# Optimization experiments

Measured on AMD Instinct MI355X. Metric: run time of the kernel, lower is better.

## Reference

```python
import jax, jax.numpy as jnp
import numpy as np

CH = 128
GROUPS = 8
HEADS = 8
HEAD_DIM = CH // HEADS  # 16
EPS = 1e-5


def setup_inputs() -> dict:
    key = jax.random.key(0)
    ks = jax.random.split(key, 5)
    x = jax.random.normal(ks[0], (8, CH, 128, 128), dtype=jnp.float32)
    gn_w = jnp.ones((CH,), dtype=jnp.float32)
    gn_b = jnp.zeros((CH,), dtype=jnp.float32)
    w_in = jax.random.normal(ks[1], (CH, CH), dtype=jnp.float32) * (1.0 / np.sqrt(CH))
    b_in = jax.random.normal(ks[2], (CH,), dtype=jnp.float32) * 0.01
    w_out = jax.random.normal(ks[3], (CH, CH), dtype=jnp.float32) * (1.0 / np.sqrt(CH))
    b_out = jax.random.normal(ks[4], (CH,), dtype=jnp.float32) * 0.01
    return {"x": x, "gn_w": gn_w, "gn_b": gn_b, "w_in": w_in, "b_in": b_in,
            "w_out": w_out, "b_out": b_out}


def _group_norm(x, gamma, beta):
    b, c, H, W = x.shape
    xg = x.reshape(b, GROUPS, c // GROUPS, H, W)
    mean = xg.mean(axis=(2, 3, 4), keepdims=True)
    var = xg.var(axis=(2, 3, 4), keepdims=True)
    xg = (xg - mean) * jax.lax.rsqrt(var + EPS)
    x = xg.reshape(b, c, H, W)
    return x * gamma[None, :, None, None] + beta[None, :, None, None]


def _conv1x1(x, w, bias):
    # w: [out_c, in_c] (1x1 conv == pointwise matmul over channels)
    return jnp.einsum('oc,bchw->bohw', w, x) + bias[None, :, None, None]


def reference(x, gn_w, gn_b, w_in, b_in, w_out, b_out):
    b, c, H, W = x.shape
    h = _group_norm(x, gn_w, gn_b)
    h = _conv1x1(h, w_in, b_in)
    # reshape to [b, heads, head_dim, H*W]; attention over head_dim axis,
    # contracting the spatial axis (d = H*W) as in the original einsums
    hh = h.reshape(b, HEADS, HEAD_DIM, H * W)
    scale = HEAD_DIM ** (-0.5)
    scores = jnp.einsum('bhid,bhjd->bhij', hh, hh) * scale  # [b,heads,hd,hd]
    weights = jax.nn.softmax(scores, axis=-1)
    attn = jnp.einsum('bhij,bhjd->bhid', weights, hh)
    attn = attn.reshape(b, c, H, W)
    h = _conv1x1(attn, w_out, b_out)
    return x + h
```

## Files before the change

kernel.cpp:

```cpp
#include <hip/hip_runtime.h>


#define NPOS 16384
#define PITCH 136

typedef short short8 __attribute__((ext_vector_type(8)));
typedef float f32x4 __attribute__((ext_vector_type(4)));

__device__ __forceinline__ unsigned short f2bf(float f) {
    union { float f; unsigned u; } v; v.f = f;
    unsigned r = (v.u + 0x7fffu + ((v.u >> 16) & 1u)) >> 16;
    return (unsigned short)r;
}

__global__ __launch_bounds__(256) void k_stats(const float* __restrict__ x,
                                               float* __restrict__ stats) {
    const float4* p = (const float4*)(x + (size_t)blockIdx.x * 16384);
    int t = threadIdx.x;
    float s1 = 0.f, s2 = 0.f;
#pragma unroll
    for (int j = 0; j < 16; ++j) {
        float4 v = p[t + j * 256];
        s1 += v.x + v.y + v.z + v.w;
        s2 += v.x * v.x + v.y * v.y + v.z * v.z + v.w * v.w;
    }
    for (int off = 32; off; off >>= 1) {
        s1 += __shfl_down(s1, off);
        s2 += __shfl_down(s2, off);
    }
    __shared__ float r1[4], r2[4];
    int wv = t >> 6;
    if ((t & 63) == 0) { r1[wv] = s1; r2[wv] = s2; }
    __syncthreads();
    if (t == 0) {
        s1 = r1[0] + r1[1] + r1[2] + r1[3];
        s2 = r2[0] + r2[1] + r2[2] + r2[3];
        int bg = blockIdx.x >> 4;
        atomicAdd(&stats[bg * 2 + 0], s1);
        atomicAdd(&stats[bg * 2 + 1], s2);
    }
}

__global__ __launch_bounds__(128) void k_prep(const float* __restrict__ stats,
                                              const float* __restrict__ gn_w,
                                              const float* __restrict__ gn_b,
                                              const float* __restrict__ w_in,
                                              const float* __restrict__ b_in,
                                              float* __restrict__ vA,
                                              unsigned short* __restrict__ Asb) {
    int b = blockIdx.x, c = threadIdx.x;
    int g = c >> 4;
    float s1 = stats[(b * 8 + g) * 2 + 0];
    float s2 = stats[(b * 8 + g) * 2 + 1];
    const float invN = 1.0f / 262144.0f;
    float mean = s1 * invN;
    float var = s2 * invN - mean * mean;
    float rstd = rsqrtf(var + 1e-5f);
    float s = gn_w[c] * rstd;
    float tt = gn_b[c] - mean * s;
    __shared__ float tl[128], sl[128];
    tl[c] = tt; sl[c] = s;
    __syncthreads();
    float v = b_in[c];
    const float* wr = w_in + c * 128;
    unsigned short* ar = Asb + b * 16384 + c * 128;
#pragma unroll 8
    for (int k = 0; k < 128; k += 4) {
        float4 w = *(const float4*)&wr[k];
        v += w.x * tl[k] + w.y * tl[k + 1] + w.z * tl[k + 2] + w.w * tl[k + 3];
        ushort4 o;
        o.x = f2bf(w.x * sl[k]);     o.y = f2bf(w.y * sl[k + 1]);
        o.z = f2bf(w.z * sl[k + 2]); o.w = f2bf(w.w * sl[k + 3]);
        *(ushort4*)&ar[k] = o;
    }
    vA[b * 128 + c] = v;
}

__global__ __launch_bounds__(256, 4) void k_gemm1_scores(const float* __restrict__ x,
                                                         const unsigned short* __restrict__ Asb,
                                                         const float* __restrict__ vA,
                                                         unsigned short* __restrict__ h1t,
                                                         float* __restrict__ Sg) {
    __shared__ unsigned short Xt[128 * PITCH];
    __shared__ float v_s[128];

    const int t = threadIdx.x;
    const int lane = t & 63, wv = t >> 6;
    const int q = lane >> 4, i16 = lane & 15;
    const int b = blockIdx.x >> 7;
    const int p0 = (blockIdx.x & 127) << 7;

    if (t < 128) v_s[t] = vA[b * 128 + t];

    const float* xb = x + (size_t)b * (128 * NPOS) + p0;
#pragma unroll
    for (int i = 0; i < 16; ++i) {
        int p = ((i & 1) << 6) + lane;
        int kq = (wv << 3) + (i >> 1);
        const float* col = xb + (size_t)(kq * 4) * NPOS + p;
        float a0 = col[0];
        float a1 = col[NPOS];
        float a2 = col[2 * NPOS];
        float a3 = col[3 * NPOS];
        ushort4 o; o.x = f2bf(a0); o.y = f2bf(a1); o.z = f2bf(a2); o.w = f2bf(a3);
        *(ushort4*)&Xt[p * PITCH + kq * 4] = o;
    }
    __syncthreads();

    f32x4 acc[2][8];
#pragma unroll
    for (int a = 0; a < 2; ++a)
#pragma unroll
        for (int pt = 0; pt < 8; ++pt) acc[a][pt] = (f32x4){0.f, 0.f, 0.f, 0.f};

    const unsigned short* Ab = Asb + b * 16384;
#pragma unroll
    for (int ks = 0; ks < 4; ++ks) {
        short8 a0 = *(const short8*)&Ab[(wv * 32 + i16) * 128 + ks * 32 + q * 8];
        short8 a1 = *(const short8*)&Ab[(wv * 32 + 16 + i16) * 128 + ks * 32 + q * 8];
#pragma unroll
        for (int pt = 0; pt < 8; ++pt) {
            short8 bb = *(const short8*)&Xt[(pt * 16 + i16) * PITCH + ks * 32 + q * 8];
            acc[0][pt] = __builtin_amdgcn_mfma_f32_16x16x32_bf16(a0, bb, acc[0][pt], 0, 0, 0);
            acc[1][pt] = __builtin_amdgcn_mfma_f32_16x16x32_bf16(a1, bb, acc[1][pt], 0, 0, 0);
        }
    }
    __syncthreads();

    unsigned short* Hs = Xt;
    unsigned short* hb = h1t + ((size_t)b * NPOS + p0) * 128;
#pragma unroll
    for (int a = 0; a < 2; ++a) {
        int cb = wv * 32 + a * 16 + q * 4;
#pragma unroll
        for (int pt = 0; pt < 8; ++pt) {
            int p = pt * 16 + i16;
            ushort4 o;
            o.x = f2bf(acc[a][pt][0] + v_s[cb + 0]);
            o.y = f2bf(acc[a][pt][1] + v_s[cb + 1]);
            o.z = f2bf(acc[a][pt][2] + v_s[cb + 2]);
            o.w = f2bf(acc[a][pt][3] + v_s[cb + 3]);
            Hs[(cb + 0) * PITCH + p] = o.x;
            Hs[(cb + 1) * PITCH + p] = o.y;
            Hs[(cb + 2) * PITCH + p] = o.z;
            Hs[(cb + 3) * PITCH + p] = o.w;
            *(ushort4*)&hb[(size_t)p * 128 + cb] = o;
        }
    }
    __syncthreads();

#pragma unroll
    for (int hh = 0; hh < 2; ++hh) {
        int h = wv * 2 + hh;
        f32x4 sacc = (f32x4){0.f, 0.f, 0.f, 0.f};
#pragma unroll
        for (int ks = 0; ks < 4; ++ks) {
            short8 f = *(const short8*)&Hs[(h * 16 + i16) * PITCH + ks * 32 + q * 8];
            sacc = __builtin_amdgcn_mfma_f32_16x16x32_bf16(f, f, sacc, 0, 0, 0);
        }
        float* sg = Sg + (b * 8 + h) * 256;
#pragma unroll
        for (int r = 0; r < 4; ++r)
            atomicAdd(&sg[(q * 4 + r) * 16 + i16], sacc[r]);
    }
}

__global__ __launch_bounds__(256) void k_softmax_weff(const float* __restrict__ Sg,
                                                      const float* __restrict__ w_out,
                                                      unsigned short* __restrict__ weffb) {
    int b = blockIdx.x >> 3;
    int ch = blockIdx.x & 7;
    int t = threadIdx.x;
    __shared__ float W[2048];
    if (t < 128) {
        const float* row = Sg + b * 2048 + t * 16;
        float v[16];
        float m = -1e30f;
#pragma unroll
        for (int j = 0; j < 16; ++j) { v[j] = row[j] * 0.25f; m = fmaxf(m, v[j]); }
        float sum = 0.f;
#pragma unroll
        for (int j = 0; j < 16; ++j) { v[j] = __expf(v[j] - m); sum += v[j]; }
        float inv = 1.0f / sum;
#pragma unroll
        for (int j = 0; j < 16; ++j) W[t * 16 + j] = v[j] * inv;
    }
    __syncthreads();
    unsigned short* wo = weffb + b * 16384 + ch * 2048;
#pragma unroll
    for (int n = 0; n < 8; ++n) {
        int idx = t + n * 256;
        int c = idx >> 7, k = idx & 127;
        int h = k >> 4, j = k & 15;
        const float* wr = w_out + (ch * 16 + c) * 128 + h * 16;
        const float* Wr = W + h * 256 + j;
        float a = 0.f;
#pragma unroll
        for (int i = 0; i < 16; ++i) a += wr[i] * Wr[i * 16];
        wo[idx] = f2bf(a);
    }
}

__global__ __launch_bounds__(256, 4) void k_attn_out(const float* __restrict__ x,
                                                     const unsigned short* __restrict__ weffb,
                                                     const unsigned short* __restrict__ h1t,
                                                     const float* __restrict__ b_out,
                                                     float* __restrict__ out) {
    __shared__ float bo_s[128];
    const int t = threadIdx.x;
    const int lane = t & 63, wv = t >> 6;
    const int q = lane >> 4, i16 = lane & 15;
    const int b = blockIdx.x >> 7;
    const int p0 = (blockIdx.x & 127) << 7;

    if (t < 128) bo_s[t] = b_out[t];
    __syncthreads();

    f32x4 acc[2][8];
#pragma unroll
    for (int a = 0; a < 2; ++a)
#pragma unroll
        for (int pt = 0; pt < 8; ++pt) acc[a][pt] = (f32x4){0.f, 0.f, 0.f, 0.f};

    const unsigned short* Wb = weffb + b * 16384;
    const unsigned short* Hb = h1t + ((size_t)b * NPOS + p0) * 128;
#pragma unroll
    for (int ks = 0; ks < 4; ++ks) {
        short8 a0 = *(const short8*)&Wb[(wv * 32 + i16) * 128 + ks * 32 + q * 8];
        short8 a1 = *(const short8*)&Wb[(wv * 32 + 16 + i16) * 128 + ks * 32 + q * 8];
#pragma unroll
        for (int pt = 0; pt < 8; ++pt) {
            short8 bb = *(const short8*)&Hb[(size_t)(pt * 16 + i16) * 128 + ks * 32 + q * 8];
            acc[0][pt] = __builtin_amdgcn_mfma_f32_16x16x32_bf16(a0, bb, acc[0][pt], 0, 0, 0);
            acc[1][pt] = __builtin_amdgcn_mfma_f32_16x16x32_bf16(a1, bb, acc[1][pt], 0, 0, 0);
        }
    }

    const float* xb = x + (size_t)b * (128 * NPOS) + p0;
    float* ob = out + (size_t)b * (128 * NPOS) + p0;
#pragma unroll
    for (int a = 0; a < 2; ++a) {
        int cb = wv * 32 + a * 16 + q * 4;
#pragma unroll
        for (int pt = 0; pt < 8; ++pt) {
            int p = pt * 16 + i16;
#pragma unroll
            for (int r = 0; r < 4; ++r) {
                int c = cb + r;
                ob[(size_t)c * NPOS + p] = acc[a][pt][r] + bo_s[c] + xb[(size_t)c * NPOS + p];
            }
        }
    }
}

extern "C" void kernel_launch(void* const* d_in, const int* in_sizes, int n_in,
                              void* d_out, int out_size, void* d_ws, size_t ws_size,
                              hipStream_t stream) {
    const float* x    = (const float*)d_in[0];
    const float* gn_w = (const float*)d_in[1];
    const float* gn_b = (const float*)d_in[2];
    const float* w_in = (const float*)d_in[3];
    const float* b_in = (const float*)d_in[4];
    const float* w_out= (const float*)d_in[5];
    const float* b_out= (const float*)d_in[6];
    float* out = (float*)d_out;

    char* ws = (char*)d_ws;
    float* stats          = (float*)(ws + 0);
    float* Sg             = (float*)(ws + 512);
    float* vA             = (float*)(ws + 66048);
    unsigned short* Asb   = (unsigned short*)(ws + 70144);
    unsigned short* weffb = (unsigned short*)(ws + 332288);
    unsigned short* h1t   = (unsigned short*)(ws + 594432);

    hipMemsetAsync(d_ws, 0, 66048, stream);
    k_stats<<<dim3(1024), dim3(256), 0, stream>>>(x, stats);
    k_prep<<<dim3(8), dim3(128), 0, stream>>>(stats, gn_w, gn_b, w_in, b_in, vA, Asb);
    k_gemm1_scores<<<dim3(1024), dim3(256), 0, stream>>>(x, Asb, vA, h1t, Sg);
    k_softmax_weff<<<dim3(64), dim3(256), 0, stream>>>(Sg, w_out, weffb);
    k_attn_out<<<dim3(1024), dim3(256), 0, stream>>>(x, weffb, h1t, b_out, out);
}
```

Measured before the change: 201.8 us.

## Fold whole pipeline into Gram matrix of x plus one fused per-batch matrix

Replaces the stats, h1 materialisation and score kernels with a single pass that computes the channel Gram matrix X·Xᵀ and channel sums of x using MFMA. A small per-batch kernel derives the group-norm statistics from the Gram diagonal and sums, forms the scores algebraically (A·G·Aᵀ plus bias terms), applies softmax, and folds w_out·softmax·A into one matrix M and bias. The output kernel then does a single GEMM of M against x plus the residual. This removes the bf16 h1t round trip through global memory and one full GEMM pass, and swizzles the shared-memory layout. In exchange it adds heavy atomic accumulation into G and possible precision loss, since the Gram matrix is quantised to bf16 and the variance comes from E[x²]−mean².

```diff
diff --git a/kernel.cpp b/kernel.cpp
--- a/kernel.cpp
+++ b/kernel.cpp
@@ -2,7 +2,6 @@
 
 
 #define NPOS 16384
-#define PITCH 136
 
 typedef short short8 __attribute__((ext_vector_type(8)));
 typedef float f32x4 __attribute__((ext_vector_type(4)));
@@ -12,77 +11,261 @@
     unsigned r = (v.u + 0x7fffu + ((v.u >> 16) & 1u)) >> 16;
     return (unsigned short)r;
 }
-
-__global__ __launch_bounds__(256) void k_stats(const float* __restrict__ x,
-                                               float* __restrict__ stats) {
-    const float4* p = (const float4*)(x + (size_t)blockIdx.x * 16384);
-    int t = threadIdx.x;
-    float s1 = 0.f, s2 = 0.f;
-#pragma unroll
-    for (int j = 0; j < 16; ++j) {
-        float4 v = p[t + j * 256];
-        s1 += v.x + v.y + v.z + v.w;
-        s2 += v.x * v.x + v.y * v.y + v.z * v.z + v.w * v.w;
-    }
-    for (int off = 32; off; off >>= 1) {
-        s1 += __shfl_down(s1, off);
-        s2 += __shfl_down(s2, off);
-    }
-    __shared__ float r1[4], r2[4];
-    int wv = t >> 6;
-    if ((t & 63) == 0) { r1[wv] = s1; r2[wv] = s2; }
-    __syncthreads();
-    if (t == 0) {
-        s1 = r1[0] + r1[1] + r1[2] + r1[3];
-        s2 = r2[0] + r2[1] + r2[2] + r2[3];
-        int bg = blockIdx.x >> 4;
-        atomicAdd(&stats[bg * 2 + 0], s1);
-        atomicAdd(&stats[bg * 2 + 1], s2);
-    }
-}
-
-__global__ __launch_bounds__(128) void k_prep(const float* __restrict__ stats,
-                                              const float* __restrict__ gn_w,
-                                              const float* __restrict__ gn_b,
-                                              const float* __restrict__ w_in,
-                                              const float* __restrict__ b_in,
-                                              float* __restrict__ vA,
-                                              unsigned short* __restrict__ Asb) {
-    int b = blockIdx.x, c = threadIdx.x;
-    int g = c >> 4;
-    float s1 = stats[(b * 8 + g) * 2 + 0];
-    float s2 = stats[(b * 8 + g) * 2 + 1];
-    const float invN = 1.0f / 262144.0f;
-    float mean = s1 * invN;
-    float var = s2 * invN - mean * mean;
-    float rstd = rsqrtf(var + 1e-5f);
-    float s = gn_w[c] * rstd;
-    float tt = gn_b[c] - mean * s;
-    __shared__ float tl[128], sl[128];
-    tl[c] = tt; sl[c] = s;
-    __syncthreads();
-    float v = b_in[c];
-    const float* wr = w_in + c * 128;
-    unsigned short* ar = Asb + b * 16384 + c * 128;
-#pragma unroll 8
-    for (int k = 0; k < 128; k += 4) {
-        float4 w = *(const float4*)&wr[k];
-        v += w.x * tl[k] + w.y * tl[k + 1] + w.z * tl[k + 2] + w.w * tl[k + 3];
+__device__ __forceinline__ float bf2f(unsigned short u) {
+    union { unsigned u; float f; } v; v.u = ((unsigned)u) << 16;
+    return v.f;
+}
+
+__global__ __launch_bounds__(256, 2) void k_gram(const float* __restrict__ x,
+                                                 float* __restrict__ G,
+                                                 float* __restrict__ mv) {
+    __shared__ unsigned short Xs[128 * 256];
+
+    const int t = threadIdx.x;
+    const int lane = t & 63, wv = t >> 6;
+    const int q = lane >> 4, i16 = lane & 15;
+    const int b = blockIdx.x >> 6;
+    const int d0 = (blockIdx.x & 63) << 8;
+
+    const float* xb = x + (size_t)b * (128 * NPOS) + d0;
+#pragma unroll
+    for (int i = 0; i < 32; ++i) {
+        int idx = t + i * 256;
+        int c = idx >> 6, d4 = idx & 63;
+        float4 v = *((const float4*)(xb + (size_t)c * NPOS) + d4);
         ushort4 o;
-        o.x = f2bf(w.x * sl[k]);     o.y = f2bf(w.y * sl[k + 1]);
-        o.z = f2bf(w.z * sl[k + 2]); o.w = f2bf(w.w * sl[k + 3]);
-        *(ushort4*)&ar[k] = o;
-    }
-    vA[b * 128 + c] = v;
-}
-
-__global__ __launch_bounds__(256, 4) void k_gemm1_scores(const float* __restrict__ x,
-                                                         const unsigned short* __restrict__ Asb,
-                                                         const float* __restrict__ vA,
-                                                         unsigned short* __restrict__ h1t,
-                                                         float* __restrict__ Sg) {
-    __shared__ unsigned short Xt[128 * PITCH];
-    __shared__ float v_s[128];
+        o.x = f2bf(v.x); o.y = f2bf(v.y); o.z = f2bf(v.z); o.w = f2bf(v.w);
+        int g = d4 >> 1;
+        int sg = g ^ (c & 7);
+        *(ushort4*)&Xs[c * 256 + (sg << 3) + ((d4 & 1) << 2)] = o;
+    }
+    __syncthreads();
+
+    f32x4 acc[2][8];
+    f32x4 macc[2];
+#pragma unroll
+    for (int a = 0; a < 2; ++a) {
+        macc[a] = (f32x4){0.f, 0.f, 0.f, 0.f};
+#pragma unroll
+        for (int ct = 0; ct < 8; ++ct) acc[a][ct] = (f32x4){0.f, 0.f, 0.f, 0.f};
+    }
+    const short8 ones = {(short)0x3F80, (short)0x3F80, (short)0x3F80, (short)0x3F80,
+                         (short)0x3F80, (short)0x3F80, (short)0x3F80, (short)0x3F80};
+    const int r0 = wv * 32 + i16, r1 = r0 + 16;
+#pragma unroll
+    for (int ks = 0; ks < 8; ++ks) {
+        int g = ks * 4 + q;
+        short8 a0 = *(const short8*)&Xs[r0 * 256 + ((g ^ (r0 & 7)) << 3)];
+        short8 a1 = *(const short8*)&Xs[r1 * 256 + ((g ^ (r1 & 7)) << 3)];
+        macc[0] = __builtin_amdgcn_mfma_f32_16x16x32_bf16(a0, ones, macc[0], 0, 0, 0);
+        macc[1] = __builtin_amdgcn_mfma_f32_16x16x32_bf16(a1, ones, macc[1], 0, 0, 0);
+#pragma unroll
+        for (int ct = 0; ct < 8; ++ct) {
+            int rb = ct * 16 + i16;
+            short8 bb = *(const short8*)&Xs[rb * 256 + ((g ^ (rb & 7)) << 3)];
+            acc[0][ct] = __builtin_amdgcn_mfma_f32_16x16x32_bf16(a0, bb, acc[0][ct], 0, 0, 0);
+            acc[1][ct] = __builtin_amdgcn_mfma_f32_16x16x32_bf16(a1, bb, acc[1][ct], 0, 0, 0);
+        }
+    }
+
+    float* Gb = G + b * 16384;
+#pragma unroll
+    for (int a = 0; a < 2; ++a) {
+        int rb = wv * 32 + a * 16 + q * 4;
+#pragma unroll
+        for (int ct = 0; ct < 8; ++ct)
+#pragma unroll
+            for (int r = 0; r < 4; ++r)
+                atomicAdd(&Gb[(rb + r) * 128 + ct * 16 + i16], acc[a][ct][r]);
+        if (i16 == 0) {
+#pragma unroll
+            for (int r = 0; r < 4; ++r)
+                atomicAdd(&mv[b * 128 + rb + r], macc[a][r]);
+        }
+    }
+}
+
+__global__ __launch_bounds__(512, 1) void k_fold(
+    const float* __restrict__ G, const float* __restrict__ mv,
+    const float* __restrict__ gn_w, const float* __restrict__ gn_b,
+    const float* __restrict__ w_in, const float* __restrict__ b_in,
+    const float* __restrict__ w_out, const float* __restrict__ b_out,
+    unsigned short* __restrict__ Mb, float* __restrict__ bias2) {
+    __shared__ unsigned short As[128 * 136];
+    __shared__ float T2f[128 * 132];
+    __shared__ float sW[8 * 16 * 16];
+    __shared__ float sm[128], ss[128], st[128], sv[128], su[128], t2v[128];
+    __shared__ float red[8][128];
+
+    unsigned short* Ts = (unsigned short*)T2f;
+
+    const int t = threadIdx.x;
+    const int lane = t & 63, wv = t >> 6;
+    const int q = lane >> 4, i16 = lane & 15;
+    const int b = blockIdx.x;
+    const float* Gb = G + b * 16384;
+
+    if (t < 128) sm[t] = mv[b * 128 + t];
+    __syncthreads();
+    if (t < 128) {
+        int g = t >> 4;
+        float s1 = 0.f, s2 = 0.f;
+#pragma unroll
+        for (int k = 0; k < 16; ++k) {
+            int c = g * 16 + k;
+            s1 += sm[c];
+            s2 += Gb[c * 128 + c];
+        }
+        const float invN = 1.0f / 262144.0f;
+        float mean = s1 * invN;
+        float var = s2 * invN - mean * mean;
+        float rstd = rsqrtf(var + 1e-5f);
+        float s = gn_w[t] * rstd;
+        ss[t] = s;
+        st[t] = gn_b[t] - mean * s;
+    }
+    __syncthreads();
+
+    {
+        int c = t & 127, quarter = t >> 7;
+        float v = 0.f, u = 0.f;
+        const float* wr = w_in + c * 128 + quarter * 32;
+        unsigned short* ar = &As[c * 136 + quarter * 32];
+#pragma unroll
+        for (int k = 0; k < 32; ++k) {
+            int kg = quarter * 32 + k;
+            float w = wr[k];
+            float a = w * ss[kg];
+            ar[k] = f2bf(a);
+            v += w * st[kg];
+            u += a * sm[kg];
+        }
+        red[quarter][c] = v;
+        red[4 + quarter][c] = u;
+    }
+    for (int idx = t; idx < 16384; idx += 512)
+        Ts[(idx >> 7) * 136 + (idx & 127)] = f2bf(Gb[idx]);
+    __syncthreads();
+    if (t < 128) {
+        sv[t] = b_in[t] + red[0][t] + red[1][t] + red[2][t] + red[3][t];
+        su[t] = red[4][t] + red[5][t] + red[6][t] + red[7][t];
+    }
+    __syncthreads();
+
+    f32x4 tacc[8];
+#pragma unroll
+    for (int ct = 0; ct < 8; ++ct) tacc[ct] = (f32x4){0.f, 0.f, 0.f, 0.f};
+    const int rA = wv * 16 + i16;
+#pragma unroll
+    for (int ks = 0; ks < 4; ++ks) {
+        short8 af = *(const short8*)&As[rA * 136 + ks * 32 + q * 8];
+#pragma unroll
+        for (int ct = 0; ct < 8; ++ct) {
+            short8 gb = *(const short8*)&Ts[(ct * 16 + i16) * 136 + ks * 32 + q * 8];
+            tacc[ct] = __builtin_amdgcn_mfma_f32_16x16x32_bf16(af, gb, tacc[ct], 0, 0, 0);
+        }
+    }
+    __syncthreads();
+#pragma unroll
+    for (int ct = 0; ct < 8; ++ct)
+#pragma unroll
+        for (int r = 0; r < 4; ++r)
+            Ts[(wv * 16 + q * 4 + r) * 136 + ct * 16 + i16] = f2bf(tacc[ct][r]);
+    __syncthreads();
+
+    {
+        f32x4 sacc = (f32x4){0.f, 0.f, 0.f, 0.f};
+#pragma unroll
+        for (int ks = 0; ks < 4; ++ks) {
+            short8 tf = *(const short8*)&Ts[rA * 136 + ks * 32 + q * 8];
+            short8 af = *(const short8*)&As[rA * 136 + ks * 32 + q * 8];
+            sacc = __builtin_amdgcn_mfma_f32_16x16x32_bf16(tf, af, sacc, 0, 0, 0);
+        }
+        int J = wv * 16 + i16;
+        float vJ = sv[J], uJ = su[J];
+#pragma unroll
+        for (int r = 0; r < 4; ++r) {
+            int I = wv * 16 + q * 4 + r;
+            float val = (sacc[r] + su[I] * vJ + sv[I] * uJ + 16384.f * sv[I] * vJ) * 0.25f;
+            float mx = val;
+#pragma unroll
+            for (int msk = 1; msk < 16; msk <<= 1) mx = fmaxf(mx, __shfl_xor(mx, msk));
+            float e = __expf(val - mx);
+            float sum = e;
+#pragma unroll
+            for (int msk = 1; msk < 16; msk <<= 1) sum += __shfl_xor(sum, msk);
+            sW[(wv * 16 + q * 4 + r) * 16 + i16] = e / sum;
+        }
+    }
+    __syncthreads();
+
+    {
+        int o = t & 127, quarter = t >> 7;
+        int h = o >> 4, ii = o & 15;
+        float a32[32];
+#pragma unroll
+        for (int kk = 0; kk < 32; ++kk) a32[kk] = 0.f;
+#pragma unroll
+        for (int j = 0; j < 16; ++j) {
+            float wj = sW[(h * 16 + ii) * 16 + j];
+            const ushort4* ar4 = (const ushort4*)&As[(h * 16 + j) * 136 + quarter * 32];
+#pragma unroll
+            for (int k4 = 0; k4 < 8; ++k4) {
+                ushort4 vv = ar4[k4];
+                a32[k4 * 4 + 0] += wj * bf2f(vv.x);
+                a32[k4 * 4 + 1] += wj * bf2f(vv.y);
+                a32[k4 * 4 + 2] += wj * bf2f(vv.z);
+                a32[k4 * 4 + 3] += wj * bf2f(vv.w);
+            }
+        }
+#pragma unroll
+        for (int kk = 0; kk < 32; ++kk) T2f[o * 132 + quarter * 32 + kk] = a32[kk];
+        if (t < 128) {
+            float a = 0.f;
+#pragma unroll
+            for (int j = 0; j < 16; ++j) a += sW[(h * 16 + ii) * 16 + j] * sv[h * 16 + j];
+            t2v[t] = a;
+        }
+    }
+    __syncthreads();
+
+    {
+        int c = t & 127, quarter = t >> 7;
+        float accM[32];
+#pragma unroll
+        for (int kk = 0; kk < 32; ++kk) accM[kk] = 0.f;
+        const float* wor = w_out + c * 128;
+        for (int o = 0; o < 128; ++o) {
+            float w = wor[o];
+            const float4* t2r = (const float4*)&T2f[o * 132 + quarter * 32];
+#pragma unroll
+            for (int k4 = 0; k4 < 8; ++k4) {
+                float4 vv = t2r[k4];
+                accM[k4 * 4 + 0] += w * vv.x;
+                accM[k4 * 4 + 1] += w * vv.y;
+                accM[k4 * 4 + 2] += w * vv.z;
+                accM[k4 * 4 + 3] += w * vv.w;
+            }
+        }
+        unsigned short* mrow = Mb + (size_t)b * 16384 + c * 128 + quarter * 32;
+#pragma unroll
+        for (int kk = 0; kk < 32; ++kk) mrow[kk] = f2bf(accM[kk]);
+        if (t < 128) {
+            float a = b_out[t];
+            const float* wr = w_out + t * 128;
+#pragma unroll
+            for (int o = 0; o < 128; ++o) a += wr[o] * t2v[o];
+            bias2[b * 128 + t] = a;
+        }
+    }
+}
+
+__global__ __launch_bounds__(256, 4) void k_out(const float* __restrict__ x,
+                                                const unsigned short* __restrict__ Mb,
+                                                const float* __restrict__ bias2,
+                                                float* __restrict__ out) {
+    __shared__ unsigned short Xt[128 * 128];
+    __shared__ float b2s[128];
 
     const int t = threadIdx.x;
     const int lane = t & 63, wv = t >> 6;
@@ -90,7 +273,7 @@
     const int b = blockIdx.x >> 7;
     const int p0 = (blockIdx.x & 127) << 7;
 
-    if (t < 128) v_s[t] = vA[b * 128 + t];
+    if (t < 128) b2s[t] = bias2[b * 128 + t];
 
     const float* xb = x + (size_t)b * (128 * NPOS) + p0;
 #pragma unroll
@@ -103,7 +286,9 @@
         float a2 = col[2 * NPOS];
         float a3 = col[3 * NPOS];
         ushort4 o; o.x = f2bf(a0); o.y = f2bf(a1); o.z = f2bf(a2); o.w = f2bf(a3);
-        *(ushort4*)&Xt[p * PITCH + kq * 4] = o;
+        int g = kq >> 1;
+        int sg = g ^ (p & 7);
+        *(ushort4*)&Xt[p * 128 + (sg << 3) + ((kq & 1) << 2)] = o;
     }
     __syncthreads();
 
@@ -113,141 +298,32 @@
 #pragma unroll
         for (int pt = 0; pt < 8; ++pt) acc[a][pt] = (f32x4){0.f, 0.f, 0.f, 0.f};
 
-    const unsigned short* Ab = Asb + b * 16384;
+    const unsigned short* Mrow = Mb + (size_t)b * 16384;
 #pragma unroll
     for (int ks = 0; ks < 4; ++ks) {
-        short8 a0 = *(const short8*)&Ab[(wv * 32 + i16) * 128 + ks * 32 + q * 8];
-        short8 a1 = *(const short8*)&Ab[(wv * 32 + 16 + i16) * 128 + ks * 32 + q * 8];
+        short8 a0 = *(const short8*)&Mrow[(wv * 32 + i16) * 128 + ks * 32 + q * 8];
+        short8 a1 = *(const short8*)&Mrow[(wv * 32 + 16 + i16) * 128 + ks * 32 + q * 8];
+        int g = ks * 4 + q;
 #pragma unroll
         for (int pt = 0; pt < 8; ++pt) {
-            short8 bb = *(const short8*)&Xt[(pt * 16 + i16) * PITCH + ks * 32 + q * 8];
+            int pr = pt * 16 + i16;
+            short8 bb = *(const short8*)&Xt[pr * 128 + ((g ^ (pr & 7)) << 3)];
             acc[0][pt] = __builtin_amdgcn_mfma_f32_16x16x32_bf16(a0, bb, acc[0][pt], 0, 0, 0);
             acc[1][pt] = __builtin_amdgcn_mfma_f32_16x16x32_bf16(a1, bb, acc[1][pt], 0, 0, 0);
         }
     }
-    __syncthreads();
-
-    unsigned short* Hs = Xt;
-    unsigned short* hb = h1t + ((size_t)b * NPOS + p0) * 128;
+
+    float* ob = out + (size_t)b * (128 * NPOS) + p0;
 #pragma unroll
     for (int a = 0; a < 2; ++a) {
         int cb = wv * 32 + a * 16 + q * 4;
 #pragma unroll
         for (int pt = 0; pt < 8; ++pt) {
             int p = pt * 16 + i16;
-            ushort4 o;
-            o.x = f2bf(acc[a][pt][0] + v_s[cb + 0]);
-            o.y = f2bf(acc[a][pt][1] + v_s[cb + 1]);
-            o.z = f2bf(acc[a][pt][2] + v_s[cb + 2]);
-            o.w = f2bf(acc[a][pt][3] + v_s[cb + 3]);
-            Hs[(cb + 0) * PITCH + p] = o.x;
-            Hs[(cb + 1) * PITCH + p] = o.y;
-            Hs[(cb + 2) * PITCH + p] = o.z;
-            Hs[(cb + 3) * PITCH + p] = o.w;
-            *(ushort4*)&hb[(size_t)p * 128 + cb] = o;
-        }
-    }
-    __syncthreads();
-
-#pragma unroll
-    for (int hh = 0; hh < 2; ++hh) {
-        int h = wv * 2 + hh;
-        f32x4 sacc = (f32x4){0.f, 0.f, 0.f, 0.f};
-#pragma unroll
-        for (int ks = 0; ks < 4; ++ks) {
-            short8 f = *(const short8*)&Hs[(h * 16 + i16) * PITCH + ks * 32 + q * 8];
-            sacc = __builtin_amdgcn_mfma_f32_16x16x32_bf16(f, f, sacc, 0, 0, 0);
-        }
-        float* sg = Sg + (b * 8 + h) * 256;
-#pragma unroll
-        for (int r = 0; r < 4; ++r)
-            atomicAdd(&sg[(q * 4 + r) * 16 + i16], sacc[r]);
-    }
-}
-
-__global__ __launch_bounds__(256) void k_softmax_weff(const float* __restrict__ Sg,
-                                                      const float* __restrict__ w_out,
-                                                      unsigned short* __restrict__ weffb) {
-    int b = blockIdx.x >> 3;
-    int ch = blockIdx.x & 7;
-    int t = threadIdx.x;
-    __shared__ float W[2048];
-    if (t < 128) {
-        const float* row = Sg + b * 2048 + t * 16;
-        float v[16];
-        float m = -1e30f;
-#pragma unroll
-        for (int j = 0; j < 16; ++j) { v[j] = row[j] * 0.25f; m = fmaxf(m, v[j]); }
-        float sum = 0.f;
-#pragma unroll
-        for (int j = 0; j < 16; ++j) { v[j] = __expf(v[j] - m); sum += v[j]; }
-        float inv = 1.0f / sum;
-#pragma unroll
-        for (int j = 0; j < 16; ++j) W[t * 16 + j] = v[j] * inv;
-    }
-    __syncthreads();
-    unsigned short* wo = weffb + b * 16384 + ch * 2048;
-#pragma unroll
-    for (int n = 0; n < 8; ++n) {
-        int idx = t + n * 256;
-        int c = idx >> 7, k = idx & 127;
-        int h = k >> 4, j = k & 15;
-        const float* wr = w_out + (ch * 16 + c) * 128 + h * 16;
-        const float* Wr = W + h * 256 + j;
-        float a = 0.f;
-#pragma unroll
-        for (int i = 0; i < 16; ++i) a += wr[i] * Wr[i * 16];
-        wo[idx] = f2bf(a);
-    }
-}
-
-__global__ __launch_bounds__(256, 4) void k_attn_out(const float* __restrict__ x,
-                                                     const unsigned short* __restrict__ weffb,
-                                                     const unsigned short* __restrict__ h1t,
-                                                     const float* __restrict__ b_out,
-                                                     float* __restrict__ out) {
-    __shared__ float bo_s[128];
-    const int t = threadIdx.x;
-    const int lane = t & 63, wv = t >> 6;
-    const int q = lane >> 4, i16 = lane & 15;
-    const int b = blockIdx.x >> 7;
-    const int p0 = (blockIdx.x & 127) << 7;
-
-    if (t < 128) bo_s[t] = b_out[t];
-    __syncthreads();
-
-    f32x4 acc[2][8];
-#pragma unroll
-    for (int a = 0; a < 2; ++a)
-#pragma unroll
-        for (int pt = 0; pt < 8; ++pt) acc[a][pt] = (f32x4){0.f, 0.f, 0.f, 0.f};
-
-    const unsigned short* Wb = weffb + b * 16384;
-    const unsigned short* Hb = h1t + ((size_t)b * NPOS + p0) * 128;
-#pragma unroll
-    for (int ks = 0; ks < 4; ++ks) {
-        short8 a0 = *(const short8*)&Wb[(wv * 32 + i16) * 128 + ks * 32 + q * 8];
-        short8 a1 = *(const short8*)&Wb[(wv * 32 + 16 + i16) * 128 + ks * 32 + q * 8];
-#pragma unroll
-        for (int pt = 0; pt < 8; ++pt) {
-            short8 bb = *(const short8*)&Hb[(size_t)(pt * 16 + i16) * 128 + ks * 32 + q * 8];
-            acc[0][pt] = __builtin_amdgcn_mfma_f32_16x16x32_bf16(a0, bb, acc[0][pt], 0, 0, 0);
-            acc[1][pt] = __builtin_amdgcn_mfma_f32_16x16x32_bf16(a1, bb, acc[1][pt], 0, 0, 0);
-        }
-    }
-
-    const float* xb = x + (size_t)b * (128 * NPOS) + p0;
-    float* ob = out + (size_t)b * (128 * NPOS) + p0;
-#pragma unroll
-    for (int a = 0; a < 2; ++a) {
-        int cb = wv * 32 + a * 16 + q * 4;
-#pragma unroll
-        for (int pt = 0; pt < 8; ++pt) {
-            int p = pt * 16 + i16;
 #pragma unroll
             for (int r = 0; r < 4; ++r) {
                 int c = cb + r;
-                ob[(size_t)c * NPOS + p] = acc[a][pt][r] + bo_s[c] + xb[(size_t)c * NPOS + p];
+                ob[(size_t)c * NPOS + p] = acc[a][pt][r] + b2s[c] + xb[(size_t)c * NPOS + p];
             }
         }
     }
@@ -266,17 +342,14 @@
     float* out = (float*)d_out;
 
     char* ws = (char*)d_ws;
-    float* stats          = (float*)(ws + 0);
-    float* Sg             = (float*)(ws + 512);
-    float* vA             = (float*)(ws + 66048);
-    unsigned short* Asb   = (unsigned short*)(ws + 70144);
-    unsigned short* weffb = (unsigned short*)(ws + 332288);
-    unsigned short* h1t   = (unsigned short*)(ws + 594432);
-
-    hipMemsetAsync(d_ws, 0, 66048, stream);
-    k_stats<<<dim3(1024), dim3(256), 0, stream>>>(x, stats);
-    k_prep<<<dim3(8), dim3(128), 0, stream>>>(stats, gn_w, gn_b, w_in, b_in, vA, Asb);
-    k_gemm1_scores<<<dim3(1024), dim3(256), 0, stream>>>(x, Asb, vA, h1t, Sg);
-    k_softmax_weff<<<dim3(64), dim3(256), 0, stream>>>(Sg, w_out, weffb);
-    k_attn_out<<<dim3(1024), dim3(256), 0, stream>>>(x, weffb, h1t, b_out, out);
-}
+    float* G              = (float*)(ws + 0);
+    float* mv             = (float*)(ws + 524288);
+    float* bias2          = (float*)(ws + 528384);
+    unsigned short* Mb    = (unsigned short*)(ws + 532480);
+
+    hipMemsetAsync(d_ws, 0, 528384, stream);
+    k_gram<<<dim3(512), dim3(256), 0, stream>>>(x, G, mv);
+    k_fold<<<dim3(8), dim3(512), 0, stream>>>(G, mv, gn_w, gn_b, w_in, b_in,
+                                              w_out, b_out, Mb, bias2);
+    k_out<<<dim3(1024), dim3(256), 0, stream>>>(x, Mb, bias2, out);
+}
```

Result: no change. 204.1 us (+1.1%).
